# Performance work log

Hardware: AMD Instinct MI355X
Metric: run time of the kernel (lower is better)

The kernel has to match this reference:

```python
import math
import jax, jax.numpy as jnp
import numpy as np

B_SZ, N_TOK, D_INNER, S_STATE = 4, 1024, 384, 16
DT_MAX = 0.15


def setup_inputs() -> dict:
    key = jax.random.key(0)
    ks = jax.random.split(key, 10)
    dt_init = math.log(math.exp(0.1) - 1.0)  # softplus^-1(0.1)
    x = jax.random.normal(ks[0], (B_SZ, N_TOK, D_INNER), dtype=jnp.float32)
    dt_self_W = jax.random.uniform(ks[1], (D_INNER, D_INNER), minval=-1e-4, maxval=1e-4)
    dt_self_b = jnp.full((D_INNER,), dt_init, dtype=jnp.float32)
    dt_diff_W = jax.random.uniform(ks[2], (D_INNER, D_INNER), minval=-1e-4, maxval=1e-4)
    dt_diff_b = jnp.full((D_INNER,), dt_init, dtype=jnp.float32)
    B_W = jax.random.normal(ks[3], (D_INNER, S_STATE)) / math.sqrt(D_INNER)
    C_real_W = jax.random.normal(ks[4], (D_INNER, S_STATE)) / math.sqrt(D_INNER)
    C_imag_W = jax.random.normal(ks[5], (D_INNER, S_STATE)) / math.sqrt(D_INNER)
    D_param = jnp.ones((D_INNER,), dtype=jnp.float32)
    A_log = jnp.broadcast_to(jnp.log(jnp.arange(1, S_STATE + 1, dtype=jnp.float32))[None, :], (D_INNER, S_STATE))
    lap = jnp.array([[0.0, 1.0, 0.0], [1.0, -4.0, 1.0], [0.0, 1.0, 0.0]], dtype=jnp.float32) * 0.1
    conv_w = jnp.broadcast_to(lap[None, None], (D_INNER, 1, 3, 3)) + 0.01 * jax.random.normal(ks[6], (D_INNER, 1, 3, 3))
    reaction_alpha = 0.01 * jax.random.normal(ks[7], (1, 1, D_INNER, 1))
    reaction_beta = 0.01 * jax.random.normal(ks[8], (1, 1, D_INNER, 1))
    return {
        'x': x, 'dt_self_W': dt_self_W, 'dt_self_b': dt_self_b,
        'dt_diff_W': dt_diff_W, 'dt_diff_b': dt_diff_b,
        'B_W': B_W, 'C_real_W': C_real_W, 'C_imag_W': C_imag_W,
        'D_param': D_param, 'A_log': A_log, 'conv_w': conv_w,
        'reaction_alpha': reaction_alpha, 'reaction_beta': reaction_beta,
        'K_steps': 2,
    }


def _laplacian(h, conv_w, H, W):
    # h: (B, N, D, S) -> depthwise 3x3 conv with replicate pad over the HxW grid
    B, N, D, S = h.shape
    hs = h.transpose(0, 3, 2, 1).reshape(B * S, D, H, W)
    hp = jnp.pad(hs, ((0, 0), (0, 0), (1, 1), (1, 1)), mode='edge')
    lap = jax.lax.conv_general_dilated(
        hp, conv_w, window_strides=(1, 1), padding='VALID',
        feature_group_count=D, dimension_numbers=('NCHW', 'OIHW', 'NCHW'))
    return lap.reshape(B, S, D, N).transpose(0, 3, 2, 1)


def reference(x, dt_self_W, dt_self_b, dt_diff_W, dt_diff_b, B_W, C_real_W,
              C_imag_W, D_param, A_log, conv_w, reaction_alpha, reaction_beta,
              K_steps):
    B, N, D = x.shape
    H = Wg = int(math.sqrt(N))
    A = -jax.nn.softplus(A_log)  # (D, S)
    delta_s = jnp.minimum(jax.nn.softplus(x @ dt_self_W.T + dt_self_b), DT_MAX)[..., None]
    delta_d = jnp.minimum(jax.nn.softplus(x @ dt_diff_W.T + dt_diff_b), DT_MAX)[..., None]
    B_mat = x @ B_W          # (B, N, S)
    C_real = x @ C_real_W    # (B, N, S)
    C_imag = x @ C_imag_W    # (B, N, S)
    mamba_input = jnp.einsum('bnd,bns->bnds', x, B_mat)
    h_real = mamba_input
    h_imag = jnp.zeros_like(h_real)
    dt = 1.0 / K_steps
    A_exp = A[None, None]  # (1,1,D,S)
    for _ in range(K_steps):
        f1_real = delta_s * (A_exp * h_real + mamba_input)
        f1_imag = delta_s * (A_exp * h_imag)
        lap_real = _laplacian(h_real, conv_w, H, Wg)
        lap_imag = _laplacian(h_imag, conv_w, H, Wg)
        f2_real = delta_d * -lap_imag
        f2_imag = delta_d * lap_real
        reaction_scale = reaction_alpha - reaction_beta * (h_real ** 2 + h_imag ** 2)
        h_real = h_real + dt * (f1_real + f2_real + h_real * reaction_scale)
        h_imag = h_imag + dt * (f1_imag + f2_imag + h_imag * reaction_scale)
    y = (jnp.einsum('bnds,bns->bnd', h_real, C_real)
         + jnp.einsum('bnds,bns->bnd', h_imag, C_imag)
         + x * D_param)
    return y
```

## Files before the change

kernel.cpp:

```cpp
#include <hip/hip_runtime.h>
#include <hip/hip_fp16.h>
#include <math.h>

#define B_SZ    4
#define N_TOKC  1024
#define D_INNER 384
#define S_STATE 16
#define DT_MAX_V 0.15f
#define PLANE   (B_SZ * N_TOKC)
#define DN      ((size_t)B_SZ * D_INNER * N_TOKC)

typedef __attribute__((ext_vector_type(8))) short bf16x8;
typedef __attribute__((ext_vector_type(4))) float f32x4;

__device__ __forceinline__ float softplusf(float z) {
    return fmaxf(z, 0.f) + log1pf(expf(-fabsf(z)));
}

__device__ __forceinline__ unsigned short f2bf(float f) {
    unsigned u = __float_as_uint(f);
    unsigned r = (u + 0x7FFFu + ((u >> 16) & 1u)) >> 16;
    return (unsigned short)r;
}

__device__ __forceinline__ unsigned packh2(float hr, float hi) {
    __half2 h = __floats2half2_rn(hr, hi);
    union { __half2 h; unsigned u; } c; c.h = h; return c.u;
}
__device__ __forceinline__ __half2 uph2(unsigned u) {
    union { unsigned u; __half2 h; } c; c.u = u; return c.h;
}

__device__ __forceinline__ size_t frag_off(int T, int kb, int q, int l16) {
    return ((size_t)((T * 12 + kb) * 4 + q)) * 128 + l16 * 8;
}

__device__ __forceinline__ bf16x8 pack8(const float* v) {
    bf16x8 o;
#pragma unroll
    for (int e = 0; e < 8; e++) o[e] = (short)f2bf(v[e]);
    return o;
}

__global__ __launch_bounds__(256) void k_prep(
    const float* __restrict__ x, const float* __restrict__ Ws, const float* __restrict__ Wd,
    const float* __restrict__ BW, const float* __restrict__ CrW, const float* __restrict__ CiW,
    float* __restrict__ x_t, unsigned short* __restrict__ xp,
    unsigned short* __restrict__ Wdtp, unsigned short* __restrict__ Wbcp)
{
    const int t = threadIdx.x;
    const int bx = blockIdx.x;
    if (bx < 1536) {
        __shared__ __align__(16) float tile[32][36];
        const int tok0 = (bx & 127) * 32;
        const int d0   = (bx >> 7) * 32;
        const int b = tok0 >> 10, n0 = tok0 & 1023;
        {
            const int r = t >> 3, c4 = (t & 7) * 4;
            const float4 v = *(const float4*)(x + (size_t)(tok0 + r) * D_INNER + d0 + c4);
            tile[r][c4 + 0] = v.x; tile[r][c4 + 1] = v.y;
            tile[r][c4 + 2] = v.z; tile[r][c4 + 3] = v.w;
        }
        __syncthreads();
        {
            const int dr = t >> 3, n4 = (t & 7) * 4;
            float4 o;
            o.x = tile[n4 + 0][dr]; o.y = tile[n4 + 1][dr];
            o.z = tile[n4 + 2][dr]; o.w = tile[n4 + 3][dr];
            *(float4*)(x_t + ((size_t)(b * D_INNER + d0 + dr)) * N_TOKC + n0 + n4) = o;
        }
        if (t < 128) {
            const int tt = t >> 6, q = (t >> 4) & 3, l16 = t & 15;
            const int row = tt * 16 + l16;
            float v[8];
#pragma unroll
            for (int e = 0; e < 8; e++) v[e] = tile[row][q * 8 + e];
            *(bf16x8*)(xp + frag_off((tok0 >> 4) + tt, d0 >> 5, q, l16)) = pack8(v);
        }
    } else if (bx < 1584) {
        const int vv = bx - 1536;
        const int mat = vv >= 24;
        const int dt16 = mat ? vv - 24 : vv;
        const float* W = mat ? Wd : Ws;
        unsigned short* dst = Wdtp + (size_t)mat * 147456;
#pragma unroll
        for (int it = 0; it < 3; it++) {
            const int item = t + it * 256;
            const int l16 = item & 15, q = (item >> 4) & 3, kb = item >> 6;
            const float* src = W + (size_t)(dt16 * 16 + l16) * D_INNER + kb * 32 + q * 8;
            float v[8];
            const float4 v0 = *(const float4*)(src);
            const float4 v1 = *(const float4*)(src + 4);
            v[0] = v0.x; v[1] = v0.y; v[2] = v0.z; v[3] = v0.w;
            v[4] = v1.x; v[5] = v1.y; v[6] = v1.z; v[7] = v1.w;
            *(bf16x8*)(dst + frag_off(dt16, kb, q, l16)) = pack8(v);
        }
    } else {
        const int m = bx - 1584;
        const float* W2 = (m == 0) ? BW : ((m == 1) ? CrW : CiW);
#pragma unroll
        for (int it = 0; it < 3; it++) {
            const int item = t + it * 256;
            const int l16 = item & 15, q = (item >> 4) & 3, kb = item >> 6;
            float v[8];
#pragma unroll
            for (int e = 0; e < 8; e++)
                v[e] = W2[(size_t)(kb * 32 + q * 8 + e) * S_STATE + l16];
            *(bf16x8*)(Wbcp + (size_t)m * 6144 + frag_off(0, kb, q, l16)) = pack8(v);
        }
    }
}

__global__ __launch_bounds__(256) void k_gemm(
    const unsigned short* __restrict__ xp, const unsigned short* __restrict__ Wdtp,
    const unsigned short* __restrict__ Wbcp,
    const float* __restrict__ bs, const float* __restrict__ bd,
    float* __restrict__ ds_t, float* __restrict__ dd_t,
    float* __restrict__ Bm_t, float* __restrict__ Cr_t, float* __restrict__ Ci_t)
{
    const int wave = threadIdx.x >> 6;
    const int lane = threadIdx.x & 63;
    const int quad = lane >> 4, l16 = lane & 15;

    if (blockIdx.x < 384) {
        const int dbase = (blockIdx.x >> 6) * 64;
        const int tbase = (blockIdx.x & 63) * 64;
        const int wd = (wave & 1) * 32;
        const int wt = (wave >> 1) * 32;
        const int dT0 = (dbase + wd) >> 4;
        const int tT0 = (tbase + wt) >> 4;

        f32x4 acc[2][2][2];
#pragma unroll
        for (int m = 0; m < 2; m++)
#pragma unroll
            for (int i = 0; i < 2; i++)
#pragma unroll
                for (int j = 0; j < 2; j++) acc[m][i][j] = (f32x4)0.f;

        bf16x8 a0[2][2], b0[2];
#pragma unroll
        for (int m = 0; m < 2; m++)
#pragma unroll
            for (int i = 0; i < 2; i++)
                a0[m][i] = *(const bf16x8*)(Wdtp + (size_t)m * 147456
                                            + frag_off(dT0 + i, 0, quad, l16));
#pragma unroll
        for (int j = 0; j < 2; j++)
            b0[j] = *(const bf16x8*)(xp + frag_off(tT0 + j, 0, quad, l16));

#pragma unroll 2
        for (int kb = 0; kb < 12; kb++) {
            bf16x8 a1[2][2], b1[2];
            const int kn = (kb < 11) ? kb + 1 : 11;
#pragma unroll
            for (int m = 0; m < 2; m++)
#pragma unroll
                for (int i = 0; i < 2; i++)
                    a1[m][i] = *(const bf16x8*)(Wdtp + (size_t)m * 147456
                                                + frag_off(dT0 + i, kn, quad, l16));
#pragma unroll
            for (int j = 0; j < 2; j++)
                b1[j] = *(const bf16x8*)(xp + frag_off(tT0 + j, kn, quad, l16));

#pragma unroll
            for (int m = 0; m < 2; m++)
#pragma unroll
                for (int i = 0; i < 2; i++)
#pragma unroll
                    for (int j = 0; j < 2; j++)
                        acc[m][i][j] = __builtin_amdgcn_mfma_f32_16x16x32_bf16(
                            a0[m][i], b0[j], acc[m][i][j], 0, 0, 0);

#pragma unroll
            for (int m = 0; m < 2; m++)
#pragma unroll
                for (int i = 0; i < 2; i++) a0[m][i] = a1[m][i];
#pragma unroll
            for (int j = 0; j < 2; j++) b0[j] = b1[j];
        }

#pragma unroll
        for (int m = 0; m < 2; m++) {
            const float* bias = (m == 0) ? bs : bd;
            float* out = (m == 0) ? ds_t : dd_t;
#pragma unroll
            for (int i = 0; i < 2; i++)
#pragma unroll
                for (int j = 0; j < 2; j++) {
                    const int tok = tbase + wt + j * 16 + l16;
                    const int bb = tok >> 10, n = tok & 1023;
#pragma unroll
                    for (int reg = 0; reg < 4; reg++) {
                        const int d = dbase + wd + i * 16 + quad * 4 + reg;
                        const float v = fminf(softplusf(acc[m][i][j][reg] + bias[d]), DT_MAX_V);
                        out[((size_t)(bb * D_INNER + d)) * N_TOKC + n] = v;
                    }
                }
        }
    } else {
        const int tT = (blockIdx.x - 384) * 4 + wave;
        f32x4 acc[3];
#pragma unroll
        for (int m = 0; m < 3; m++) acc[m] = (f32x4)0.f;

#pragma unroll 1
        for (int kb = 0; kb < 12; kb++) {
            const bf16x8 b = *(const bf16x8*)(xp + frag_off(tT, kb, quad, l16));
#pragma unroll
            for (int m = 0; m < 3; m++) {
                const bf16x8 a = *(const bf16x8*)(Wbcp + (size_t)m * 6144
                                                  + frag_off(0, kb, quad, l16));
                acc[m] = __builtin_amdgcn_mfma_f32_16x16x32_bf16(a, b, acc[m], 0, 0, 0);
            }
        }

        const int tok = tT * 16 + l16;
#pragma unroll
        for (int m = 0; m < 3; m++) {
            float* plane = (m == 0) ? Bm_t : ((m == 1) ? Cr_t : Ci_t);
#pragma unroll
            for (int reg = 0; reg < 4; reg++) {
                const int s = quad * 4 + reg;
                plane[(size_t)s * PLANE + tok] = acc[m][reg];
            }
        }
    }
}

__global__ __launch_bounds__(256) void k_ssm(
    const float* __restrict__ x_t, const float* __restrict__ conv_w, const float* __restrict__ A_log,
    const float* __restrict__ ralpha, const float* __restrict__ rbeta, const float* __restrict__ Dp,
    const float* __restrict__ ds_t, const float* __restrict__ dd_t,
    const float* __restrict__ Bm_t, const float* __restrict__ Cr_t, const float* __restrict__ Ci_t,
    float* __restrict__ y_part)
{
    const int sg = blockIdx.x;
    const int d  = blockIdx.y;
    const int b  = blockIdx.z;
    const int t  = threadIdx.x;
    const int c  = t & 31;
    const int g  = t >> 5;
    const int r0 = g * 4;

    __shared__ unsigned pl[4][34 * 34];

    float w[9];
#pragma unroll
    for (int i = 0; i < 9; i++) w[i] = conv_w[d * 9 + i];
    __half2 wh[9];
#pragma unroll
    for (int i = 0; i < 9; i++) wh[i] = __float2half2_rn(w[i]);
    const float alpha = ralpha[d];
    const float beta  = rbeta[d];
    const float Dv    = Dp[d];
    float A[4];
#pragma unroll
    for (int s = 0; s < 4; s++) A[s] = -softplusf(A_log[d * S_STATE + sg * 4 + s]);

    const size_t base_dn = ((size_t)(b * D_INNER + d)) * N_TOKC;
    const size_t base_sn = (size_t)b * N_TOKC;

    float xv[4], dsv[4], ddv[4], Bmv[4][4];
    float hr[4][4], hi[4][4];
#pragma unroll
    for (int k = 0; k < 4; k++) {
        const int n = (r0 + k) * 32 + c;
        xv[k]  = x_t [base_dn + n];
        dsv[k] = ds_t[base_dn + n];
        ddv[k] = dd_t[base_dn + n];
#pragma unroll
        for (int s = 0; s < 4; s++) {
            Bmv[k][s] = Bm_t[(size_t)(sg * 4 + s) * PLANE + base_sn + n];
            hr[k][s]  = xv[k] * Bmv[k][s];
        }
    }

    const int wslot = (r0 + 1) * 34 + (c + 1);
    const int rbase = r0 * 34 + c;

#pragma unroll
    for (int s = 0; s < 4; s++) {
#pragma unroll
        for (int k = 0; k < 4; k++)
            pl[s][wslot + k * 34] = __float_as_uint(hr[k][s]);
        if (g == 0) pl[s][c + 1]           = __float_as_uint(hr[0][s]);
        if (g == 7) pl[s][33 * 34 + c + 1] = __float_as_uint(hr[3][s]);
        if (c == 0) {
#pragma unroll
            for (int k = 0; k < 4; k++) pl[s][(r0 + 1 + k) * 34] = __float_as_uint(hr[k][s]);
            if (g == 0) pl[s][0]       = __float_as_uint(hr[0][s]);
            if (g == 7) pl[s][33 * 34] = __float_as_uint(hr[3][s]);
        }
        if (c == 31) {
#pragma unroll
            for (int k = 0; k < 4; k++) pl[s][(r0 + 1 + k) * 34 + 33] = __float_as_uint(hr[k][s]);
            if (g == 0) pl[s][33]           = __float_as_uint(hr[0][s]);
            if (g == 7) pl[s][33 * 34 + 33] = __float_as_uint(hr[3][s]);
        }
    }
    __syncthreads();

    float lr0[4][4];
#pragma unroll
    for (int s = 0; s < 4; s++) {
        float fr[6][3];
#pragma unroll
        for (int rr = 0; rr < 6; rr++)
#pragma unroll
            for (int bb = 0; bb < 3; bb++)
                fr[rr][bb] = __uint_as_float(pl[s][rbase + rr * 34 + bb]);
#pragma unroll
        for (int k = 0; k < 4; k++) {
            float ar = 0.f;
#pragma unroll
            for (int a = 0; a < 3; a++)
#pragma unroll
                for (int bb = 0; bb < 3; bb++)
                    ar = fmaf(w[a * 3 + bb], fr[k + a][bb], ar);
            lr0[k][s] = ar;
        }
    }
    __syncthreads();

#pragma unroll
    for (int k = 0; k < 4; k++)
#pragma unroll
        for (int s = 0; s < 4; s++) {
            const float hrv = hr[k][s];
            const float u   = xv[k] * Bmv[k][s];
            const float f1r = dsv[k] * fmaf(A[s], hrv, u);
            const float rs  = fmaf(-beta, hrv * hrv, alpha);
            hr[k][s] = hrv + 0.5f * (f1r + hrv * rs);
            hi[k][s] = 0.5f * ddv[k] * lr0[k][s];
        }

#pragma unroll
    for (int s = 0; s < 4; s++) {
#pragma unroll
        for (int k = 0; k < 4; k++)
            pl[s][wslot + k * 34] = packh2(hr[k][s], hi[k][s]);
        if (g == 0) pl[s][c + 1]           = packh2(hr[0][s], hi[0][s]);
        if (g == 7) pl[s][33 * 34 + c + 1] = packh2(hr[3][s], hi[3][s]);
        if (c == 0) {
#pragma unroll
            for (int k = 0; k < 4; k++) pl[s][(r0 + 1 + k) * 34] = packh2(hr[k][s], hi[k][s]);
            if (g == 0) pl[s][0]       = packh2(hr[0][s], hi[0][s]);
            if (g == 7) pl[s][33 * 34] = packh2(hr[3][s], hi[3][s]);
        }
        if (c == 31) {
#pragma unroll
            for (int k = 0; k < 4; k++) pl[s][(r0 + 1 + k) * 34 + 33] = packh2(hr[k][s], hi[k][s]);
            if (g == 0) pl[s][33]           = packh2(hr[0][s], hi[0][s]);
            if (g == 7) pl[s][33 * 34 + 33] = packh2(hr[3][s], hi[3][s]);
        }
    }
    __syncthreads();

    float lr1[4][4], li1[4][4];
#pragma unroll
    for (int s = 0; s < 4; s++) {
        __half2 f2[6][3];
#pragma unroll
        for (int rr = 0; rr < 6; rr++)
#pragma unroll
            for (int bb = 0; bb < 3; bb++)
                f2[rr][bb] = uph2(pl[s][rbase + rr * 34 + bb]);
#pragma unroll
        for (int k = 0; k < 4; k++) {
            __half2 ac = __float2half2_rn(0.f);
#pragma unroll
            for (int a = 0; a < 3; a++)
#pragma unroll
                for (int bb = 0; bb < 3; bb++)
                    ac = __hfma2(wh[a * 3 + bb], f2[k + a][bb], ac);
            lr1[k][s] = __low2float(ac);
            li1[k][s] = __high2float(ac);
        }
    }

#pragma unroll
    for (int k = 0; k < 4; k++)
#pragma unroll
        for (int s = 0; s < 4; s++) {
            const float hrv = hr[k][s], hiv = hi[k][s];
            const float u   = xv[k] * Bmv[k][s];
            const float f1r = dsv[k] * fmaf(A[s], hrv, u);
            const float f1i = dsv[k] * (A[s] * hiv);
            const float f2r = -ddv[k] * li1[k][s];
            const float f2i =  ddv[k] * lr1[k][s];
            const float q   = fmaf(hrv, hrv, hiv * hiv);
            const float rs  = fmaf(-beta, q, alpha);
            hr[k][s] = hrv + 0.5f * (f1r + f2r + hrv * rs);
            hi[k][s] = hiv + 0.5f * (f1i + f2i + hiv * rs);
        }

#pragma unroll
    for (int k = 0; k < 4; k++) {
        const int n = (r0 + k) * 32 + c;
        float yp = 0.f;
#pragma unroll
        for (int s = 0; s < 4; s++) {
            const size_t po = (size_t)(sg * 4 + s) * PLANE + base_sn + n;
            yp = fmaf(hr[k][s], Cr_t[po], yp);
            yp = fmaf(hi[k][s], Ci_t[po], yp);
        }
        if (sg == 0) yp = fmaf(xv[k], Dv, yp);
        y_part[((size_t)((sg * B_SZ + b) * D_INNER + d)) * N_TOKC + n] = yp;
    }
}

__global__ __launch_bounds__(256) void k_reduce(
    const float* __restrict__ y_part, float* __restrict__ y)
{
    const int d0 = blockIdx.x * 32;
    const int n0 = blockIdx.y * 32;
    const int b  = blockIdx.z;
    const int t  = threadIdx.x;
    __shared__ __align__(16) float tile[32][36];

    const int dr = t >> 3, nc4 = (t & 7) * 4;
    float4 acc = make_float4(0.f, 0.f, 0.f, 0.f);
#pragma unroll
    for (int sg = 0; sg < 4; sg++) {
        const float4 v = *(const float4*)(y_part
            + ((size_t)((sg * B_SZ + b) * D_INNER + d0 + dr)) * N_TOKC + n0 + nc4);
        acc.x += v.x; acc.y += v.y; acc.z += v.z; acc.w += v.w;
    }
    *(float4*)&tile[dr][nc4] = acc;
    __syncthreads();

    const int nr = t >> 3, dc4 = (t & 7) * 4;
    float4 o;
    o.x = tile[dc4 + 0][nr];
    o.y = tile[dc4 + 1][nr];
    o.z = tile[dc4 + 2][nr];
    o.w = tile[dc4 + 3][nr];
    *(float4*)(y + ((size_t)(b * N_TOKC + n0 + nr)) * D_INNER + d0 + dc4) = o;
}

extern "C" void kernel_launch(void* const* d_in, const int* in_sizes, int n_in,
                              void* d_out, int out_size, void* d_ws, size_t ws_size,
                              hipStream_t stream)
{
    const float* x    = (const float*)d_in[0];
    const float* Ws   = (const float*)d_in[1];
    const float* bsb  = (const float*)d_in[2];
    const float* Wd   = (const float*)d_in[3];
    const float* bdb  = (const float*)d_in[4];
    const float* BW   = (const float*)d_in[5];
    const float* CrW  = (const float*)d_in[6];
    const float* CiW  = (const float*)d_in[7];
    const float* Dp   = (const float*)d_in[8];
    const float* Alog = (const float*)d_in[9];
    const float* cw   = (const float*)d_in[10];
    const float* ra   = (const float*)d_in[11];
    const float* rb   = (const float*)d_in[12];
    float* y = (float*)d_out;

    float* ws     = (float*)d_ws;
    float* ds_t   = ws;
    float* dd_t   = ds_t + DN;
    float* x_t    = dd_t + DN;
    float* Bm_t   = x_t + DN;
    float* Cr_t   = Bm_t + (size_t)S_STATE * PLANE;
    float* Ci_t   = Cr_t + (size_t)S_STATE * PLANE;
    float* y_part = Ci_t + (size_t)S_STATE * PLANE;

    unsigned short* xp   = (unsigned short*)y_part;
    unsigned short* Wdtp = xp + (size_t)256 * 12 * 4 * 128;
    unsigned short* Wbcp = Wdtp + (size_t)2 * 147456;

    k_prep<<<dim3(1587), 256, 0, stream>>>(x, Ws, Wd, BW, CrW, CiW, x_t, xp, Wdtp, Wbcp);
    k_gemm<<<dim3(448), 256, 0, stream>>>(xp, Wdtp, Wbcp, bsb, bdb,
                                          ds_t, dd_t, Bm_t, Cr_t, Ci_t);
    k_ssm<<<dim3(4, D_INNER, B_SZ), 256, 0, stream>>>(x_t, cw, Alog, ra, rb, Dp,
                                                      ds_t, dd_t, Bm_t, Cr_t, Ci_t, y_part);
    k_reduce<<<dim3(12, 32, 4), 256, 0, stream>>>(y_part, y);
}
```

Baseline: 173.9 us.

## Restructure SSM stencil: clamped-index halos, fp16 packed first pass, fused output

The SSM kernel drops the padded 34x34 halo planes and instead computes clamped neighbour indices for replicate padding, storing an unpadded 33-stride plane. This removes the edge-thread halo writes. The first Laplacian now packs two states per half2 in fp16 instead of using fp32, which halves shared memory traffic and sync rounds but lowers precision. The final update is fused with the C projection, and the A=-softplus(A_log) table is precomputed in the prep kernel. Together these cut shared-memory work, register pressure and per-block transcendental work.

```diff
diff --git a/kernel.cpp b/kernel.cpp
--- a/kernel.cpp
+++ b/kernel.cpp
@@ -23,8 +23,8 @@
     return (unsigned short)r;
 }
 
-__device__ __forceinline__ unsigned packh2(float hr, float hi) {
-    __half2 h = __floats2half2_rn(hr, hi);
+__device__ __forceinline__ unsigned packh2(float a, float b) {
+    __half2 h = __floats2half2_rn(a, b);
     union { __half2 h; unsigned u; } c; c.h = h; return c.u;
 }
 __device__ __forceinline__ __half2 uph2(unsigned u) {
@@ -45,8 +45,10 @@
 __global__ __launch_bounds__(256) void k_prep(
     const float* __restrict__ x, const float* __restrict__ Ws, const float* __restrict__ Wd,
     const float* __restrict__ BW, const float* __restrict__ CrW, const float* __restrict__ CiW,
+    const float* __restrict__ A_log,
     float* __restrict__ x_t, unsigned short* __restrict__ xp,
-    unsigned short* __restrict__ Wdtp, unsigned short* __restrict__ Wbcp)
+    unsigned short* __restrict__ Wdtp, unsigned short* __restrict__ Wbcp,
+    float* __restrict__ A_tab)
 {
     const int t = threadIdx.x;
     const int bx = blockIdx.x;
@@ -95,7 +97,7 @@
             v[4] = v1.x; v[5] = v1.y; v[6] = v1.z; v[7] = v1.w;
             *(bf16x8*)(dst + frag_off(dt16, kb, q, l16)) = pack8(v);
         }
-    } else {
+    } else if (bx < 1587) {
         const int m = bx - 1584;
         const float* W2 = (m == 0) ? BW : ((m == 1) ? CrW : CiW);
 #pragma unroll
@@ -108,6 +110,9 @@
                 v[e] = W2[(size_t)(kb * 32 + q * 8 + e) * S_STATE + l16];
             *(bf16x8*)(Wbcp + (size_t)m * 6144 + frag_off(0, kb, q, l16)) = pack8(v);
         }
+    } else {
+        for (int i = t; i < D_INNER * S_STATE; i += 256)
+            A_tab[i] = -softplusf(A_log[i]);
     }
 }
 
@@ -228,8 +233,11 @@
     }
 }
 
+#define PSTRIDE 33
+#define PSIZE   (PSTRIDE * 32)
+
 __global__ __launch_bounds__(256) void k_ssm(
-    const float* __restrict__ x_t, const float* __restrict__ conv_w, const float* __restrict__ A_log,
+    const float* __restrict__ x_t, const float* __restrict__ conv_w, const float* __restrict__ A_tab,
     const float* __restrict__ ralpha, const float* __restrict__ rbeta, const float* __restrict__ Dp,
     const float* __restrict__ ds_t, const float* __restrict__ dd_t,
     const float* __restrict__ Bm_t, const float* __restrict__ Cr_t, const float* __restrict__ Ci_t,
@@ -243,25 +251,22 @@
     const int g  = t >> 5;
     const int r0 = g * 4;
 
-    __shared__ unsigned pl[4][34 * 34];
-
-    float w[9];
-#pragma unroll
-    for (int i = 0; i < 9; i++) w[i] = conv_w[d * 9 + i];
+    __shared__ unsigned pl[4 * PSIZE];
+
     __half2 wh[9];
 #pragma unroll
-    for (int i = 0; i < 9; i++) wh[i] = __float2half2_rn(w[i]);
+    for (int i = 0; i < 9; i++) wh[i] = __float2half2_rn(conv_w[d * 9 + i]);
     const float alpha = ralpha[d];
     const float beta  = rbeta[d];
     const float Dv    = Dp[d];
     float A[4];
 #pragma unroll
-    for (int s = 0; s < 4; s++) A[s] = -softplusf(A_log[d * S_STATE + sg * 4 + s]);
+    for (int s = 0; s < 4; s++) A[s] = A_tab[d * S_STATE + sg * 4 + s];
 
     const size_t base_dn = ((size_t)(b * D_INNER + d)) * N_TOKC;
     const size_t base_sn = (size_t)b * N_TOKC;
 
-    float xv[4], dsv[4], ddv[4], Bmv[4][4];
+    float xv[4], dsv[4], ddv[4], u[4][4];
     float hr[4][4], hi[4][4];
 #pragma unroll
     for (int k = 0; k < 4; k++) {
@@ -271,142 +276,120 @@
         ddv[k] = dd_t[base_dn + n];
 #pragma unroll
         for (int s = 0; s < 4; s++) {
-            Bmv[k][s] = Bm_t[(size_t)(sg * 4 + s) * PLANE + base_sn + n];
-            hr[k][s]  = xv[k] * Bmv[k][s];
-        }
-    }
-
-    const int wslot = (r0 + 1) * 34 + (c + 1);
-    const int rbase = r0 * 34 + c;
-
-#pragma unroll
-    for (int s = 0; s < 4; s++) {
+            u[k][s]  = xv[k] * Bm_t[(size_t)(sg * 4 + s) * PLANE + base_sn + n];
+            hr[k][s] = u[k][s];
+        }
+    }
+
+    int tapw[6][3];
+    {
+        const int cm = (c > 0)  ? c - 1 : 0;
+        const int cp = (c < 31) ? c + 1 : 31;
+        const int rtop = (r0 > 0)  ? r0 - 1 : 0;
+        const int rbot = (r0 < 28) ? r0 + 4 : 31;
+        int rowb[6];
+        rowb[0] = rtop * PSTRIDE;
+#pragma unroll
+        for (int k = 0; k < 4; k++) rowb[k + 1] = (r0 + k) * PSTRIDE;
+        rowb[5] = rbot * PSTRIDE;
+#pragma unroll
+        for (int rr = 0; rr < 6; rr++) {
+            tapw[rr][0] = rowb[rr] + cm;
+            tapw[rr][1] = rowb[rr] + c;
+            tapw[rr][2] = rowb[rr] + cp;
+        }
+    }
+    const int ws0 = r0 * PSTRIDE + c;
+
+#pragma unroll
+    for (int p = 0; p < 2; p++)
 #pragma unroll
         for (int k = 0; k < 4; k++)
-            pl[s][wslot + k * 34] = __float_as_uint(hr[k][s]);
-        if (g == 0) pl[s][c + 1]           = __float_as_uint(hr[0][s]);
-        if (g == 7) pl[s][33 * 34 + c + 1] = __float_as_uint(hr[3][s]);
-        if (c == 0) {
-#pragma unroll
-            for (int k = 0; k < 4; k++) pl[s][(r0 + 1 + k) * 34] = __float_as_uint(hr[k][s]);
-            if (g == 0) pl[s][0]       = __float_as_uint(hr[0][s]);
-            if (g == 7) pl[s][33 * 34] = __float_as_uint(hr[3][s]);
-        }
-        if (c == 31) {
-#pragma unroll
-            for (int k = 0; k < 4; k++) pl[s][(r0 + 1 + k) * 34 + 33] = __float_as_uint(hr[k][s]);
-            if (g == 0) pl[s][33]           = __float_as_uint(hr[0][s]);
-            if (g == 7) pl[s][33 * 34 + 33] = __float_as_uint(hr[3][s]);
-        }
-    }
+            pl[p * PSIZE + ws0 + k * PSTRIDE] = packh2(hr[k][2 * p], hr[k][2 * p + 1]);
     __syncthreads();
 
-    float lr0[4][4];
-#pragma unroll
-    for (int s = 0; s < 4; s++) {
-        float fr[6][3];
+#pragma unroll
+    for (int p = 0; p < 2; p++) {
+        __half2 tp[6][3];
 #pragma unroll
         for (int rr = 0; rr < 6; rr++)
 #pragma unroll
-            for (int bb = 0; bb < 3; bb++)
-                fr[rr][bb] = __uint_as_float(pl[s][rbase + rr * 34 + bb]);
-#pragma unroll
-        for (int k = 0; k < 4; k++) {
-            float ar = 0.f;
-#pragma unroll
-            for (int a = 0; a < 3; a++)
-#pragma unroll
-                for (int bb = 0; bb < 3; bb++)
-                    ar = fmaf(w[a * 3 + bb], fr[k + a][bb], ar);
-            lr0[k][s] = ar;
-        }
-    }
-    __syncthreads();
-
-#pragma unroll
-    for (int k = 0; k < 4; k++)
-#pragma unroll
-        for (int s = 0; s < 4; s++) {
-            const float hrv = hr[k][s];
-            const float u   = xv[k] * Bmv[k][s];
-            const float f1r = dsv[k] * fmaf(A[s], hrv, u);
-            const float rs  = fmaf(-beta, hrv * hrv, alpha);
-            hr[k][s] = hrv + 0.5f * (f1r + hrv * rs);
-            hi[k][s] = 0.5f * ddv[k] * lr0[k][s];
-        }
-
-#pragma unroll
-    for (int s = 0; s < 4; s++) {
-#pragma unroll
-        for (int k = 0; k < 4; k++)
-            pl[s][wslot + k * 34] = packh2(hr[k][s], hi[k][s]);
-        if (g == 0) pl[s][c + 1]           = packh2(hr[0][s], hi[0][s]);
-        if (g == 7) pl[s][33 * 34 + c + 1] = packh2(hr[3][s], hi[3][s]);
-        if (c == 0) {
-#pragma unroll
-            for (int k = 0; k < 4; k++) pl[s][(r0 + 1 + k) * 34] = packh2(hr[k][s], hi[k][s]);
-            if (g == 0) pl[s][0]       = packh2(hr[0][s], hi[0][s]);
-            if (g == 7) pl[s][33 * 34] = packh2(hr[3][s], hi[3][s]);
-        }
-        if (c == 31) {
-#pragma unroll
-            for (int k = 0; k < 4; k++) pl[s][(r0 + 1 + k) * 34 + 33] = packh2(hr[k][s], hi[k][s]);
-            if (g == 0) pl[s][33]           = packh2(hr[0][s], hi[0][s]);
-            if (g == 7) pl[s][33 * 34 + 33] = packh2(hr[3][s], hi[3][s]);
-        }
-    }
-    __syncthreads();
-
-    float lr1[4][4], li1[4][4];
-#pragma unroll
-    for (int s = 0; s < 4; s++) {
-        __half2 f2[6][3];
-#pragma unroll
-        for (int rr = 0; rr < 6; rr++)
-#pragma unroll
-            for (int bb = 0; bb < 3; bb++)
-                f2[rr][bb] = uph2(pl[s][rbase + rr * 34 + bb]);
+            for (int j = 0; j < 3; j++)
+                tp[rr][j] = uph2(pl[p * PSIZE + tapw[rr][j]]);
 #pragma unroll
         for (int k = 0; k < 4; k++) {
             __half2 ac = __float2half2_rn(0.f);
 #pragma unroll
             for (int a = 0; a < 3; a++)
 #pragma unroll
-                for (int bb = 0; bb < 3; bb++)
-                    ac = __hfma2(wh[a * 3 + bb], f2[k + a][bb], ac);
-            lr1[k][s] = __low2float(ac);
-            li1[k][s] = __high2float(ac);
-        }
-    }
-
-#pragma unroll
-    for (int k = 0; k < 4; k++)
-#pragma unroll
-        for (int s = 0; s < 4; s++) {
+                for (int j = 0; j < 3; j++)
+                    ac = __hfma2(wh[a * 3 + j], tp[k + a][j], ac);
+            const float lap[2] = { __low2float(ac), __high2float(ac) };
+#pragma unroll
+            for (int e = 0; e < 2; e++) {
+                const int s = 2 * p + e;
+                const float hrv = hr[k][s];
+                const float f1r = dsv[k] * fmaf(A[s], hrv, u[k][s]);
+                const float rs  = fmaf(-beta, hrv * hrv, alpha);
+                hr[k][s] = hrv + 0.5f * (f1r + hrv * rs);
+                hi[k][s] = 0.5f * ddv[k] * lap[e];
+            }
+        }
+    }
+    __syncthreads();
+
+#pragma unroll
+    for (int s = 0; s < 4; s++)
+#pragma unroll
+        for (int k = 0; k < 4; k++)
+            pl[s * PSIZE + ws0 + k * PSTRIDE] = packh2(hr[k][s], hi[k][s]);
+    __syncthreads();
+
+    float yp[4] = { 0.f, 0.f, 0.f, 0.f };
+#pragma unroll
+    for (int s = 0; s < 4; s++) {
+        float crv[4], civ[4];
+#pragma unroll
+        for (int k = 0; k < 4; k++) {
+            const size_t po = (size_t)(sg * 4 + s) * PLANE + base_sn + (r0 + k) * 32 + c;
+            crv[k] = Cr_t[po];
+            civ[k] = Ci_t[po];
+        }
+        __half2 tp[6][3];
+#pragma unroll
+        for (int rr = 0; rr < 6; rr++)
+#pragma unroll
+            for (int j = 0; j < 3; j++)
+                tp[rr][j] = uph2(pl[s * PSIZE + tapw[rr][j]]);
+#pragma unroll
+        for (int k = 0; k < 4; k++) {
+            __half2 ac = __float2half2_rn(0.f);
+#pragma unroll
+            for (int a = 0; a < 3; a++)
+#pragma unroll
+                for (int j = 0; j < 3; j++)
+                    ac = __hfma2(wh[a * 3 + j], tp[k + a][j], ac);
+            const float lapr = __low2float(ac);
+            const float lapi = __high2float(ac);
             const float hrv = hr[k][s], hiv = hi[k][s];
-            const float u   = xv[k] * Bmv[k][s];
-            const float f1r = dsv[k] * fmaf(A[s], hrv, u);
+            const float f1r = dsv[k] * fmaf(A[s], hrv, u[k][s]);
             const float f1i = dsv[k] * (A[s] * hiv);
-            const float f2r = -ddv[k] * li1[k][s];
-            const float f2i =  ddv[k] * lr1[k][s];
+            const float f2r = -ddv[k] * lapi;
+            const float f2i =  ddv[k] * lapr;
             const float q   = fmaf(hrv, hrv, hiv * hiv);
             const float rs  = fmaf(-beta, q, alpha);
-            hr[k][s] = hrv + 0.5f * (f1r + f2r + hrv * rs);
-            hi[k][s] = hiv + 0.5f * (f1i + f2i + hiv * rs);
-        }
+            const float nhr = hrv + 0.5f * (f1r + f2r + hrv * rs);
+            const float nhi = hiv + 0.5f * (f1i + f2i + hiv * rs);
+            yp[k] = fmaf(nhr, crv[k], yp[k]);
+            yp[k] = fmaf(nhi, civ[k], yp[k]);
+        }
+    }
 
 #pragma unroll
     for (int k = 0; k < 4; k++) {
-        const int n = (r0 + k) * 32 + c;
-        float yp = 0.f;
-#pragma unroll
-        for (int s = 0; s < 4; s++) {
-            const size_t po = (size_t)(sg * 4 + s) * PLANE + base_sn + n;
-            yp = fmaf(hr[k][s], Cr_t[po], yp);
-            yp = fmaf(hi[k][s], Ci_t[po], yp);
-        }
-        if (sg == 0) yp = fmaf(xv[k], Dv, yp);
-        y_part[((size_t)((sg * B_SZ + b) * D_INNER + d)) * N_TOKC + n] = yp;
+        float v = yp[k];
+        if (sg == 0) v = fmaf(xv[k], Dv, v);
+        y_part[((size_t)((sg * B_SZ + b) * D_INNER + d)) * N_TOKC + (r0 + k) * 32 + c] = v;
     }
 }
 
@@ -465,16 +448,18 @@
     float* Bm_t   = x_t + DN;
     float* Cr_t   = Bm_t + (size_t)S_STATE * PLANE;
     float* Ci_t   = Cr_t + (size_t)S_STATE * PLANE;
-    float* y_part = Ci_t + (size_t)S_STATE * PLANE;
+    float* A_tab  = Ci_t + (size_t)S_STATE * PLANE;
+    float* y_part = A_tab + (size_t)D_INNER * S_STATE;
 
     unsigned short* xp   = (unsigned short*)y_part;
     unsigned short* Wdtp = xp + (size_t)256 * 12 * 4 * 128;
     unsigned short* Wbcp = Wdtp + (size_t)2 * 147456;
 
-    k_prep<<<dim3(1587), 256, 0, stream>>>(x, Ws, Wd, BW, CrW, CiW, x_t, xp, Wdtp, Wbcp);
+    k_prep<<<dim3(1588), 256, 0, stream>>>(x, Ws, Wd, BW, CrW, CiW, Alog,
+                                           x_t, xp, Wdtp, Wbcp, A_tab);
     k_gemm<<<dim3(448), 256, 0, stream>>>(xp, Wdtp, Wbcp, bsb, bdb,
                                           ds_t, dd_t, Bm_t, Cr_t, Ci_t);
-    k_ssm<<<dim3(4, D_INNER, B_SZ), 256, 0, stream>>>(x_t, cw, Alog, ra, rb, Dp,
+    k_ssm<<<dim3(4, D_INNER, B_SZ), 256, 0, stream>>>(x_t, cw, A_tab, ra, rb, Dp,
                                                       ds_t, dd_t, Bm_t, Cr_t, Ci_t, y_part);
     k_reduce<<<dim3(12, 32, 4), 256, 0, stream>>>(y_part, y);
 }
```

Result: faster. 166.7 us (-4.2%).
